# Optimization experiments

Hardware: AMD Instinct MI355X
Metric: run time of the kernel (lower is better)

Reference implementation:

```python
import jax, jax.numpy as jnp
import numpy as np
from jax import lax

LN_EPS = 1e-5

D_MODEL, N_HEADS, HEAD_DIM, RANK, POWER_K = 1024, 16, 64, 32, 4
RIDGE_EPS, SPECTRAL_GAMMA = 1e-4, 0.99


def setup_inputs() -> dict:
    key = jax.random.key(0)
    ks = jax.random.split(key, 8)
    B, T = 4, 4096
    s = 1.0 / np.sqrt(D_MODEL)
    inp = {
        "hidden_states": jax.random.normal(ks[0], (B, T, D_MODEL), dtype=jnp.float32),
        "Wk": jax.random.normal(ks[1], (D_MODEL, N_HEADS * RANK), dtype=jnp.float32) * s,
        "Wq": jax.random.normal(ks[2], (D_MODEL, N_HEADS * RANK), dtype=jnp.float32) * s,
        "Wv": jax.random.normal(ks[3], (D_MODEL, N_HEADS * HEAD_DIM), dtype=jnp.float32) * s,
        "Wo": jax.random.normal(ks[4], (N_HEADS * HEAD_DIM, D_MODEL), dtype=jnp.float32) * s,
        "ln_scale": jnp.ones((D_MODEL,), jnp.float32),
        "ln_bias": jnp.zeros((D_MODEL,), jnp.float32),
        "gate_alpha": jnp.zeros((1,), jnp.float32),
        "log_ridge": jnp.array(np.log(RIDGE_EPS), jnp.float32),
        "log_gamma": jnp.array(np.log(SPECTRAL_GAMMA), jnp.float32),
        "prefix_len": 2048,
    }
    return inp


def _tri_solve(L, b, transpose=False):
    # solves L x = b (or L^T x = b) with lower-triangular L; batched over leading dims
    return lax.linalg.triangular_solve(L, b, left_side=True, lower=True, transpose_a=transpose)


def _build_operator(keys, values, ridge, gamma):
    # keys: (B,H,L,r), values: (B,H,L,dh)
    r = keys.shape[-1]
    G = jnp.einsum('bhlr,bhls->bhrs', keys, keys) + ridge * jnp.eye(r, dtype=keys.dtype)
    M = jnp.einsum('bhlr,bhls->bhrs', keys[:, :, 1:, :], keys[:, :, :-1, :])
    L = jnp.linalg.cholesky(G)                       # (B,H,r,r)
    U = _tri_solve(L, M)                             # L^{-1} M
    V = _tri_solve(L, jnp.swapaxes(U, -1, -2))       # L^{-1} (L^{-1}M)^T
    A_w = jnp.swapaxes(V, -1, -2)                    # L^{-1} M L^{-T}
    gamma_c = jnp.minimum(gamma, 1.0)
    sigma = jnp.linalg.svd(A_w, compute_uv=False)[..., 0]  # spectral norm
    sigma = jnp.maximum(sigma, 1e-8)
    scale = gamma_c / jnp.maximum(sigma, 1.0)
    A_w = A_w * scale[..., None, None]
    C_v = jnp.einsum('bhld,bhlr->bhdr', values, keys)       # (B,H,dh,r)
    Y = _tri_solve(L, jnp.swapaxes(C_v, -1, -2))            # L^{-1} C_v^T
    Bv_T = _tri_solve(L, Y, transpose=True)                 # G^{-1} C_v^T
    B_v = jnp.swapaxes(Bv_T, -1, -2)                        # (B,H,dh,r)
    return A_w, L, B_v


def _spectral_filter(A_w, L, B_v, queries, power_K):
    # queries: (B,H,Q,r) -> (B,H,Q,dh)
    qT = jnp.swapaxes(queries, -1, -2)      # (B,H,r,Q)
    w = _tri_solve(L, qT)                   # whiten
    for _ in range(power_K):
        w = jnp.matmul(A_w, w)
    z_hat = jnp.matmul(L, w)                # unwhiten
    out = jnp.matmul(B_v, z_hat)            # (B,H,dh,Q)
    return jnp.swapaxes(out, -1, -2)


def reference(hidden_states, Wk, Wq, Wv, Wo, ln_scale, ln_bias,
              gate_alpha, log_ridge, log_gamma, prefix_len):
    B, T, D = hidden_states.shape
    P = max(1, min(int(prefix_len), T - 1))
    mu = jnp.mean(hidden_states, axis=-1, keepdims=True)
    var = jnp.var(hidden_states, axis=-1, keepdims=True)
    normed = (hidden_states - mu) / jnp.sqrt(var + LN_EPS) * ln_scale + ln_bias
    def proj(W, dim):
        y = normed @ W
        return jnp.swapaxes(y.reshape(B, T, N_HEADS, dim), 1, 2)  # (B,H,T,dim)
    keys_all = proj(Wk, RANK)
    queries_all = proj(Wq, RANK)
    values_all = proj(Wv, HEAD_DIM)
    ridge = jnp.exp(log_ridge)
    gamma = jnp.exp(log_gamma)
    A_w, L, B_v = _build_operator(keys_all[:, :, :P, :], values_all[:, :, :P, :], ridge, gamma)
    q_out = _spectral_filter(A_w, L, B_v, queries_all[:, :, P:, :], POWER_K)
    p_out = _spectral_filter(A_w, L, B_v, keys_all[:, :, :P, :], POWER_K)
    full = jnp.concatenate([p_out, q_out], axis=2)               # (B,H,T,dh)
    full = jnp.swapaxes(full, 1, 2).reshape(B, T, N_HEADS * HEAD_DIM)
    out = full @ Wo
    return jax.nn.sigmoid(gate_alpha) * out
```

## Files before the change

kernel.cpp:

```cpp
#include <hip/hip_runtime.h>
#include <math.h>

#define D_MODEL 1024
#define TT 4096
#define NB 4
#define NH 16
#define TCH 8

typedef __attribute__((ext_vector_type(8))) short s8v;
typedef __attribute__((ext_vector_type(4))) float f4v;
typedef __attribute__((ext_vector_type(8))) unsigned short u16x8;

#define OFF_STATS ((size_t)0)
#define OFF_GP    ((size_t)(1) << 20)
#define OFF_MP    ((size_t)(3) << 20)
#define OFF_CP    ((size_t)(5) << 20)
#define OFF_FT    ((size_t)(9) << 20)
#define OFF_WKH   ((size_t)(10) << 20)
#define OFF_WKL   ((size_t)(11) << 20)
#define OFF_WQH   ((size_t)(12) << 20)
#define OFF_WQL   ((size_t)(13) << 20)
#define OFF_WVH   ((size_t)(14) << 20)
#define OFF_WVL   ((size_t)(16) << 20)
#define OFF_WOH   ((size_t)(18) << 20)
#define OFF_WOL   ((size_t)(20) << 20)
#define OFF_Y1    ((size_t)(22) << 20)
#define OFF_Y2    ((size_t)(54) << 20)
#define OFF_FH    OFF_Y2

__device__ __forceinline__ unsigned short bf16_rne(float x) {
  unsigned u = __float_as_uint(x);
  return (unsigned short)((u + 0x7fffu + ((u >> 16) & 1u)) >> 16);
}
__device__ __forceinline__ void split_bf16(float x, unsigned short& h, unsigned short& l) {
  unsigned u = __float_as_uint(x);
  unsigned r = (u + 0x7fffu + ((u >> 16) & 1u)) & 0xffff0000u;
  h = (unsigned short)(r >> 16);
  float res = x - __uint_as_float(r);
  l = bf16_rne(res);
}

__device__ __forceinline__ void gll16(unsigned short* lds, const unsigned short* g) {
  __builtin_amdgcn_global_load_lds(
      (__attribute__((address_space(1))) void*)(void*)(g),
      (__attribute__((address_space(3))) void*)(lds), 16, 0, 0);
}

__device__ __forceinline__ void xcd_swz(int gx, int gy, int& x, int& y, int& z) {
  int wg = blockIdx.x + gx * (blockIdx.y + gy * blockIdx.z);
  int k = wg & 7, j = wg >> 3;
  x = j % gx;
  int yz = k + ((j / gx) << 3);
  y = yz % gy;
  z = yz / gy;
}

__global__ __launch_bounds__(256) void ln_stats_k(const float* __restrict__ X,
                                                  float* __restrict__ stats) {
  int r = blockIdx.x;
  const float4 v = ((const float4*)(X + (size_t)r * D_MODEL))[threadIdx.x];
  float s  = v.x + v.y + v.z + v.w;
  float ss = v.x * v.x + v.y * v.y + v.z * v.z + v.w * v.w;
#pragma unroll
  for (int off = 32; off > 0; off >>= 1) {
    s  += __shfl_down(s, off, 64);
    ss += __shfl_down(ss, off, 64);
  }
  __shared__ float as_[4], bs_[4];
  int w = threadIdx.x >> 6, lane = threadIdx.x & 63;
  if (lane == 0) { as_[w] = s; bs_[w] = ss; }
  __syncthreads();
  if (threadIdx.x == 0) {
    float S  = as_[0] + as_[1] + as_[2] + as_[3];
    float SS = bs_[0] + bs_[1] + bs_[2] + bs_[3];
    float mu  = S * (1.0f / D_MODEL);
    float var = SS * (1.0f / D_MODEL) - mu * mu;
    stats[2 * (size_t)r]     = mu;
    stats[2 * (size_t)r + 1] = 1.0f / sqrtf(var + 1e-5f);
  }
}

__global__ __launch_bounds__(256) void prep_w_k(const float* __restrict__ W, int N,
                                                unsigned short* __restrict__ Thi,
                                                unsigned short* __restrict__ Tlo,
                                                int swz) {
  __shared__ float tileT[32 * 33];
  const int n0 = blockIdx.x * 32, k0 = blockIdx.y * 32;
  const int tid = threadIdx.x;
  {
    int k_l = tid >> 3, n4 = (tid & 7) << 2;
    float4 v = *(const float4*)&W[(size_t)(k0 + k_l) * N + n0 + n4];
    tileT[(n4 + 0) * 33 + k_l] = v.x;
    tileT[(n4 + 1) * 33 + k_l] = v.y;
    tileT[(n4 + 2) * 33 + k_l] = v.z;
    tileT[(n4 + 3) * 33 + k_l] = v.w;
  }
  __syncthreads();
  {
    int n_l = tid >> 3, k4 = (tid & 7) << 2;
    unsigned short h[4], l[4];
#pragma unroll
    for (int i = 0; i < 4; i++) split_bf16(tileT[n_l * 33 + k4 + i], h[i], l[i]);
    int kc = k0 + k4;
    int col = swz ? ((kc & ~63) | ((((kc >> 3) & 7) ^ (n_l & 7)) << 3) | (kc & 7)) : kc;
    *(ushort4*)&Thi[(size_t)(n0 + n_l) * 1024 + col] = make_ushort4(h[0], h[1], h[2], h[3]);
    *(ushort4*)&Tlo[(size_t)(n0 + n_l) * 1024 + col] = make_ushort4(l[0], l[1], l[2], l[3]);
  }
}

__global__ __launch_bounds__(256) void gemm_proj_k(
    const float* __restrict__ X, const float* __restrict__ stats,
    const float* __restrict__ lng, const float* __restrict__ lnb,
    const unsigned short* __restrict__ WThi, const unsigned short* __restrict__ WTlo,
    int Nw, const int* __restrict__ pref, int mode, float* __restrict__ Y) {
  int P = pref[0]; P = P < 1 ? 1 : (P > TT - 1 ? TT - 1 : P);
  int xx, yy, zz;
  xcd_swz(8, 32, xx, yy, zz);
  const int b  = zz;
  const int t0 = yy * 128;
  const int n0 = xx * 128;
  if (mode == 1) { if (t0 + 128 <= P) return; }
  else           { if (t0 >= P) return; }
  const int row0 = b * TT + t0;
  __shared__ __align__(16) unsigned short Ah[128 * 40], Al[128 * 40];
  __shared__ __align__(16) unsigned short Bh[128 * 32], Bl[128 * 32];
  __shared__ float mus[128], rss[128];
  const int tid = threadIdx.x;
  if (tid < 128) {
    mus[tid] = stats[2 * (size_t)(row0 + tid)];
    rss[tid] = stats[2 * (size_t)(row0 + tid) + 1];
  }
  const int lane = tid & 63;
  const int wid  = tid >> 6;
  const int wm = (wid >> 1) * 64, wn = (wid & 1) * 64;
  const int lm = lane & 15, lq = lane >> 4;
  const int srow = lane >> 2, scol = (lane & 3) << 3;
  f4v acc[4][4];
#pragma unroll
  for (int i = 0; i < 4; i++)
#pragma unroll
    for (int j = 0; j < 4; j++) acc[i][j] = (f4v){0.f, 0.f, 0.f, 0.f};

  for (int kt = 0; kt < D_MODEL; kt += 32) {
    __syncthreads();
#pragma unroll
    for (int s = 0; s < 2; s++) {
      int seg = wid * 2 + s;
      int brow = n0 + seg * 16 + srow;
      gll16(&Bh[seg * 512], &WThi[(size_t)brow * 1024 + kt + scol]);
      gll16(&Bl[seg * 512], &WTlo[(size_t)brow * 1024 + kt + scol]);
    }
#pragma unroll
    for (int q = 0; q < 2; q++) {
      int c = tid * 2 + q;
      int m = c >> 2, k8 = (c & 3) << 3;
      const float* src = &X[(size_t)(row0 + m) * D_MODEL + kt + k8];
      float mu = mus[m], rs = rss[m];
      u16x8 hv, lv;
#pragma unroll
      for (int i = 0; i < 8; i++) {
        float nv = (src[i] - mu) * rs * lng[kt + k8 + i] + lnb[kt + k8 + i];
        unsigned short h, l;
        split_bf16(nv, h, l);
        hv[i] = h; lv[i] = l;
      }
      *(u16x8*)&Ah[m * 40 + k8] = hv;
      *(u16x8*)&Al[m * 40 + k8] = lv;
    }
    __syncthreads();
    s8v ah[4], al[4], bh[4], bl[4];
#pragma unroll
    for (int i = 0; i < 4; i++) {
      int ar = (wm + i * 16 + lm) * 40 + lq * 8;
      int br = (wn + i * 16 + lm) * 32 + lq * 8;
      ah[i] = *(const s8v*)&Ah[ar];
      al[i] = *(const s8v*)&Al[ar];
      bh[i] = *(const s8v*)&Bh[br];
      bl[i] = *(const s8v*)&Bl[br];
    }
#pragma unroll
    for (int mi = 0; mi < 4; mi++)
#pragma unroll
      for (int ni = 0; ni < 4; ni++) {
        acc[mi][ni] = __builtin_amdgcn_mfma_f32_16x16x32_bf16(ah[mi], bh[ni], acc[mi][ni], 0, 0, 0);
        acc[mi][ni] = __builtin_amdgcn_mfma_f32_16x16x32_bf16(ah[mi], bl[ni], acc[mi][ni], 0, 0, 0);
        acc[mi][ni] = __builtin_amdgcn_mfma_f32_16x16x32_bf16(al[mi], bh[ni], acc[mi][ni], 0, 0, 0);
      }
  }
#pragma unroll
  for (int mi = 0; mi < 4; mi++) {
#pragma unroll
    for (int r = 0; r < 4; r++) {
      int t = t0 + wm + mi * 16 + lq * 4 + r;
      bool ok = (mode == 1) ? (t >= P) : (t < P);
      if (!ok) continue;
      size_t orow = (mode == 2) ? ((size_t)b * P + t) : ((size_t)b * TT + t);
#pragma unroll
      for (int ni = 0; ni < 4; ni++)
        Y[orow * Nw + n0 + wn + ni * 16 + lm] = acc[mi][ni][r];
    }
  }
}

__global__ __launch_bounds__(256) void gemm_kq_k(
    const float* __restrict__ X, const float* __restrict__ stats,
    const float* __restrict__ lng, const float* __restrict__ lnb,
    const unsigned short* __restrict__ KH, const unsigned short* __restrict__ KL,
    const unsigned short* __restrict__ QH, const unsigned short* __restrict__ QL,
    const int* __restrict__ pref, float* __restrict__ Y) {
  int P = pref[0]; P = P < 1 ? 1 : (P > TT - 1 ? TT - 1 : P);
  int xx, yy, zz;
  xcd_swz(4, 32, xx, yy, zz);
  const int b  = zz;
  const int t0 = yy * 128;
  const int n0 = xx * 128;
  const int row0 = b * TT + t0;
  const bool hasK = (t0 < P);
  const bool hasQ = (t0 + 128 > P);
  __shared__ __align__(16) unsigned short Ah[128 * 40], Al[128 * 40];
  __shared__ __align__(16) unsigned short Bh[128 * 32], Bl[128 * 32];
  __shared__ float mus[128], rss[128];
  const int tid = threadIdx.x;
  if (tid < 128) {
    mus[tid] = stats[2 * (size_t)(row0 + tid)];
    rss[tid] = stats[2 * (size_t)(row0 + tid) + 1];
  }
  const int lane = tid & 63;
  const int wid  = tid >> 6;
  const int wm = (wid >> 1) * 64, wn = (wid & 1) * 64;
  const int lm = lane & 15, lq = lane >> 4;
  const int srow = lane >> 2, scol = (lane & 3) << 3;

  for (int pass = 0; pass < 2; pass++) {
    if (pass == 0 && !hasK) continue;
    if (pass == 1 && !hasQ) continue;
    const unsigned short* WThi = pass ? QH : KH;
    const unsigned short* WTlo = pass ? QL : KL;
    f4v acc[4][4];
#pragma unroll
    for (int i = 0; i < 4; i++)
#pragma unroll
      for (int j = 0; j < 4; j++) acc[i][j] = (f4v){0.f, 0.f, 0.f, 0.f};

    for (int kt = 0; kt < D_MODEL; kt += 32) {
      __syncthreads();
#pragma unroll
      for (int s = 0; s < 2; s++) {
        int seg = wid * 2 + s;
        int brow = n0 + seg * 16 + srow;
        gll16(&Bh[seg * 512], &WThi[(size_t)brow * 1024 + kt + scol]);
        gll16(&Bl[seg * 512], &WTlo[(size_t)brow * 1024 + kt + scol]);
      }
#pragma unroll
      for (int q = 0; q < 2; q++) {
        int c = tid * 2 + q;
        int m = c >> 2, k8 = (c & 3) << 3;
        const float* src = &X[(size_t)(row0 + m) * D_MODEL + kt + k8];
        float mu = mus[m], rs = rss[m];
        u16x8 hv, lv;
#pragma unroll
        for (int i = 0; i < 8; i++) {
          float nv = (src[i] - mu) * rs * lng[kt + k8 + i] + lnb[kt + k8 + i];
          unsigned short h, l;
          split_bf16(nv, h, l);
          hv[i] = h; lv[i] = l;
        }
        *(u16x8*)&Ah[m * 40 + k8] = hv;
        *(u16x8*)&Al[m * 40 + k8] = lv;
      }
      __syncthreads();
      s8v ah[4], al[4], bh[4], bl[4];
#pragma unroll
      for (int i = 0; i < 4; i++) {
        int ar = (wm + i * 16 + lm) * 40 + lq * 8;
        int br = (wn + i * 16 + lm) * 32 + lq * 8;
        ah[i] = *(const s8v*)&Ah[ar];
        al[i] = *(const s8v*)&Al[ar];
        bh[i] = *(const s8v*)&Bh[br];
        bl[i] = *(const s8v*)&Bl[br];
      }
#pragma unroll
      for (int mi = 0; mi < 4; mi++)
#pragma unroll
        for (int ni = 0; ni < 4; ni++) {
          acc[mi][ni] = __builtin_amdgcn_mfma_f32_16x16x32_bf16(ah[mi], bh[ni], acc[mi][ni], 0, 0, 0);
          acc[mi][ni] = __builtin_amdgcn_mfma_f32_16x16x32_bf16(ah[mi], bl[ni], acc[mi][ni], 0, 0, 0);
          acc[mi][ni] = __builtin_amdgcn_mfma_f32_16x16x32_bf16(al[mi], bh[ni], acc[mi][ni], 0, 0, 0);
        }
    }
#pragma unroll
    for (int mi = 0; mi < 4; mi++) {
#pragma unroll
      for (int r = 0; r < 4; r++) {
        int t = t0 + wm + mi * 16 + lq * 4 + r;
        bool ok = pass ? (t >= P) : (t < P);
        if (!ok) continue;
#pragma unroll
        for (int ni = 0; ni < 4; ni++)
          Y[((size_t)b * TT + t) * 512 + n0 + wn + ni * 16 + lm] = acc[mi][ni][r];
      }
    }
  }
}

__global__ __launch_bounds__(256) void build_gmc_mfma_k(
    const float* __restrict__ Y1, const float* __restrict__ Y2,
    const int* __restrict__ pref,
    float* __restrict__ Gp, float* __restrict__ Mp, float* __restrict__ Cp) {
  int P = pref[0]; P = P < 1 ? 1 : (P > TT - 1 ? TT - 1 : P);
  const int c  = blockIdx.x;
  const int bh = blockIdx.y;
  const int b = bh >> 4, h = bh & 15;
  const int chunk = (P + TCH - 1) / TCH;
  const int tb = c * chunk;
  const int te = min(tb + chunk, P);

  __shared__ __align__(16) unsigned short kCh[32 * 136], kCl[32 * 136];
  __shared__ __align__(16) unsigned short kPh[32 * 136], kPl[32 * 136];
  __shared__ __align__(16) unsigned short vTh[64 * 136], vTl[64 * 136];

  const int tid = threadIdx.x;
  const int wid = tid >> 6, lane = tid & 63;
  const int lm = lane & 15, lq = lane >> 4;

  f4v acc[4];
#pragma unroll
  for (int i = 0; i < 4; i++) acc[i] = (f4v){0.f, 0.f, 0.f, 0.f};

  for (int t0 = tb; t0 < te; t0 += 128) {
    const int len = (te - t0 < 128) ? (te - t0) : 128;
    __syncthreads();
    for (int e = tid; e < 129 * 8; e += 256) {
      int row = e >> 3, j4 = (e & 7) << 2;
      int t = t0 - 1 + row;
      float4 kv = make_float4(0.f, 0.f, 0.f, 0.f);
      if (row <= len && t >= 0)
        kv = *(const float4*)&Y1[((size_t)b * TT + t) * 512 + h * 32 + j4];
      unsigned short hh[4], ll[4];
      split_bf16(kv.x, hh[0], ll[0]); split_bf16(kv.y, hh[1], ll[1]);
      split_bf16(kv.z, hh[2], ll[2]); split_bf16(kv.w, hh[3], ll[3]);
      if (row >= 1) {
#pragma unroll
        for (int q = 0; q < 4; q++) {
          kCh[(j4 + q) * 136 + row - 1] = hh[q];
          kCl[(j4 + q) * 136 + row - 1] = ll[q];
        }
      }
      if (row < 128) {
#pragma unroll
        for (int q = 0; q < 4; q++) {
          kPh[(j4 + q) * 136 + row] = hh[q];
          kPl[(j4 + q) * 136 + row] = ll[q];
        }
      }
    }
    for (int e = tid; e < 128 * 16; e += 256) {
      int row = e >> 4, dj = (e & 15) << 2;
      int t = t0 + row;
      float4 vv = make_float4(0.f, 0.f, 0.f, 0.f);
      if (row < len)
        vv = *(const float4*)&Y2[((size_t)b * P + t) * 1024 + h * 64 + dj];
      unsigned short hh[4], ll[4];
      split_bf16(vv.x, hh[0], ll[0]); split_bf16(vv.y, hh[1], ll[1]);
      split_bf16(vv.z, hh[2], ll[2]); split_bf16(vv.w, hh[3], ll[3]);
#pragma unroll
      for (int q = 0; q < 4; q++) {
        vTh[(dj + q) * 136 + row] = hh[q];
        vTl[(dj + q) * 136 + row] = ll[q];
      }
    }
    __syncthreads();

#pragma unroll
    for (int kk = 0; kk < 128; kk += 32) {
      const int off = kk + lq * 8;
      if (wid == 0) {
        s8v h0 = *(const s8v*)&kCh[(0 + lm) * 136 + off];
        s8v h1 = *(const s8v*)&kCh[(16 + lm) * 136 + off];
        s8v l0 = *(const s8v*)&kCl[(0 + lm) * 136 + off];
        s8v l1 = *(const s8v*)&kCl[(16 + lm) * 136 + off];
        acc[0] = __builtin_amdgcn_mfma_f32_16x16x32_bf16(h0, h0, acc[0], 0, 0, 0);
        acc[0] = __builtin_amdgcn_mfma_f32_16x16x32_bf16(h0, l0, acc[0], 0, 0, 0);
        acc[0] = __builtin_amdgcn_mfma_f32_16x16x32_bf16(l0, h0, acc[0], 0, 0, 0);
        acc[1] = __builtin_amdgcn_mfma_f32_16x16x32_bf16(h0, h1, acc[1], 0, 0, 0);
        acc[1] = __builtin_amdgcn_mfma_f32_16x16x32_bf16(h0, l1, acc[1], 0, 0, 0);
        acc[1] = __builtin_amdgcn_mfma_f32_16x16x32_bf16(l0, h1, acc[1], 0, 0, 0);
        acc[2] = __builtin_amdgcn_mfma_f32_16x16x32_bf16(h1, h0, acc[2], 0, 0, 0);
        acc[2] = __builtin_amdgcn_mfma_f32_16x16x32_bf16(h1, l0, acc[2], 0, 0, 0);
        acc[2] = __builtin_amdgcn_mfma_f32_16x16x32_bf16(l1, h0, acc[2], 0, 0, 0);
        acc[3] = __builtin_amdgcn_mfma_f32_16x16x32_bf16(h1, h1, acc[3], 0, 0, 0);
        acc[3] = __builtin_amdgcn_mfma_f32_16x16x32_bf16(h1, l1, acc[3], 0, 0, 0);
        acc[3] = __builtin_amdgcn_mfma_f32_16x16x32_bf16(l1, h1, acc[3], 0, 0, 0);
      } else if (wid == 1) {
        s8v ah0 = *(const s8v*)&kCh[(0 + lm) * 136 + off];
        s8v ah1 = *(const s8v*)&kCh[(16 + lm) * 136 + off];
        s8v al0 = *(const s8v*)&kCl[(0 + lm) * 136 + off];
        s8v al1 = *(const s8v*)&kCl[(16 + lm) * 136 + off];
        s8v bh0 = *(const s8v*)&kPh[(0 + lm) * 136 + off];
        s8v bh1 = *(const s8v*)&kPh[(16 + lm) * 136 + off];
        s8v bl0 = *(const s8v*)&kPl[(0 + lm) * 136 + off];
        s8v bl1 = *(const s8v*)&kPl[(16 + lm) * 136 + off];
        acc[0] = __builtin_amdgcn_mfma_f32_16x16x32_bf16(ah0, bh0, acc[0], 0, 0, 0);
        acc[0] = __builtin_amdgcn_mfma_f32_16x16x32_bf16(ah0, bl0, acc[0], 0, 0, 0);
        acc[0] = __builtin_amdgcn_mfma_f32_16x16x32_bf16(al0, bh0, acc[0], 0, 0, 0);
        acc[1] = __builtin_amdgcn_mfma_f32_16x16x32_bf16(ah0, bh1, acc[1], 0, 0, 0);
        acc[1] = __builtin_amdgcn_mfma_f32_16x16x32_bf16(ah0, bl1, acc[1], 0, 0, 0);
        acc[1] = __builtin_amdgcn_mfma_f32_16x16x32_bf16(al0, bh1, acc[1], 0, 0, 0);
        acc[2] = __builtin_amdgcn_mfma_f32_16x16x32_bf16(ah1, bh0, acc[2], 0, 0, 0);
        acc[2] = __builtin_amdgcn_mfma_f32_16x16x32_bf16(ah1, bl0, acc[2], 0, 0, 0);
        acc[2] = __builtin_amdgcn_mfma_f32_16x16x32_bf16(al1, bh0, acc[2], 0, 0, 0);
        acc[3] = __builtin_amdgcn_mfma_f32_16x16x32_bf16(ah1, bh1, acc[3], 0, 0, 0);
        acc[3] = __builtin_amdgcn_mfma_f32_16x16x32_bf16(ah1, bl1, acc[3], 0, 0, 0);
        acc[3] = __builtin_amdgcn_mfma_f32_16x16x32_bf16(al1, bh1, acc[3], 0, 0, 0);
      } else {
        const int d0 = (wid - 2) * 32;
        s8v vh0 = *(const s8v*)&vTh[(d0 + lm) * 136 + off];
        s8v vh1 = *(const s8v*)&vTh[(d0 + 16 + lm) * 136 + off];
        s8v vl0 = *(const s8v*)&vTl[(d0 + lm) * 136 + off];
        s8v vl1 = *(const s8v*)&vTl[(d0 + 16 + lm) * 136 + off];
        s8v kh0 = *(const s8v*)&kCh[(0 + lm) * 136 + off];
        s8v kh1 = *(const s8v*)&kCh[(16 + lm) * 136 + off];
        s8v kl0 = *(const s8v*)&kCl[(0 + lm) * 136 + off];
        s8v kl1 = *(const s8v*)&kCl[(16 + lm) * 136 + off];
        acc[0] = __builtin_amdgcn_mfma_f32_16x16x32_bf16(vh0, kh0, acc[0], 0, 0, 0);
        acc[0] = __builtin_amdgcn_mfma_f32_16x16x32_bf16(vh0, kl0, acc[0], 0, 0, 0);
        acc[0] = __builtin_amdgcn_mfma_f32_16x16x32_bf16(vl0, kh0, acc[0], 0, 0, 0);
        acc[1] = __builtin_amdgcn_mfma_f32_16x16x32_bf16(vh0, kh1, acc[1], 0, 0, 0);
        acc[1] = __builtin_amdgcn_mfma_f32_16x16x32_bf16(vh0, kl1, acc[1], 0, 0, 0);
        acc[1] = __builtin_amdgcn_mfma_f32_16x16x32_bf16(vl0, kh1, acc[1], 0, 0, 0);
        acc[2] = __builtin_amdgcn_mfma_f32_16x16x32_bf16(vh1, kh0, acc[2], 0, 0, 0);
        acc[2] = __builtin_amdgcn_mfma_f32_16x16x32_bf16(vh1, kl0, acc[2], 0, 0, 0);
        acc[2] = __builtin_amdgcn_mfma_f32_16x16x32_bf16(vl1, kh0, acc[2], 0, 0, 0);
        acc[3] = __builtin_amdgcn_mfma_f32_16x16x32_bf16(vh1, kh1, acc[3], 0, 0, 0);
        acc[3] = __builtin_amdgcn_mfma_f32_16x16x32_bf16(vh1, kl1, acc[3], 0, 0, 0);
        acc[3] = __builtin_amdgcn_mfma_f32_16x16x32_bf16(vl1, kh1, acc[3], 0, 0, 0);
      }
    }
  }

  if (wid < 2) {
    float* dst = (wid == 0 ? Gp : Mp) + (size_t)(c * 64 + bh) * 1024;
#pragma unroll
    for (int t = 0; t < 4; t++) {
      int i0 = (t >> 1) * 16, j0 = (t & 1) * 16;
#pragma unroll
      for (int r = 0; r < 4; r++)
        dst[(i0 + lq * 4 + r) * 32 + j0 + lm] = acc[t][r];
    }
  } else {
    float* dst = Cp + (size_t)(c * 64 + bh) * 2048;
#pragma unroll
    for (int t = 0; t < 4; t++) {
      int d0 = (wid - 2) * 32 + (t >> 1) * 16, j0 = (t & 1) * 16;
#pragma unroll
      for (int r = 0; r < 4; r++)
        dst[(d0 + lq * 4 + r) * 32 + j0 + lm] = acc[t][r];
    }
  }
}

__global__ __launch_bounds__(256) void solve_op_k(
    const float* __restrict__ Gp, const float* __restrict__ Mp,
    const float* __restrict__ Cp, const float* __restrict__ lridge,
    const float* __restrict__ lgamma, float* __restrict__ Ft) {
  __shared__ float Gs[32 * 33];
  __shared__ float Ms[32 * 32];
  __shared__ float Gi[32 * 32];
  __shared__ float W1[32 * 33];
  __shared__ float Aw[32 * 33];
  __shared__ float Nn[32 * 32];
  __shared__ float N2[32 * 32];
  __shared__ float T1[32 * 32];
  __shared__ float Cs[64 * 32];
  __shared__ float red[256];
  __shared__ float vv[32], uu[32];
  const int bh = blockIdx.x;
  const int tid = threadIdx.x;
  const float ridge = expf(lridge[0]);

  for (int e = tid; e < 1024; e += 256) {
    int i = e >> 5, j = e & 31;
    float g = 0.f, m = 0.f;
#pragma unroll
    for (int cc = 0; cc < TCH; cc++) {
      g += Gp[(size_t)(cc * 64 + bh) * 1024 + e];
      m += Mp[(size_t)(cc * 64 + bh) * 1024 + e];
    }
    if (i == j) g += ridge;
    Gs[i * 33 + j] = g;
    Ms[e] = m;
  }
  for (int e = tid; e < 2048; e += 256) {
    float s = 0.f;
#pragma unroll
    for (int cc = 0; cc < TCH; cc++) s += Cp[(size_t)(cc * 64 + bh) * 2048 + e];
    Cs[e] = s;
  }
  __syncthreads();

  for (int j = 0; j < 32; j++) {
    float d = Gs[j * 33 + j];
    __syncthreads();
    float inv = 1.0f / sqrtf(d);
    if (tid >= j && tid < 32) Gs[tid * 33 + j] *= inv;
    __syncthreads();
    int w = 31 - j;
    for (int e = tid; e < w * w; e += 256) {
      int i = j + 1 + e / w, k = j + 1 + e % w;
      Gs[i * 33 + k] -= Gs[i * 33 + j] * Gs[k * 33 + j];
    }
    __syncthreads();
  }

  if (tid < 32) {
    const int c = tid;
    for (int i = 0; i < 32; i++) W1[i * 33 + c] = (i == c) ? 1.0f : 0.0f;
    for (int i = 0; i < 32; i++) {
      float s = W1[i * 33 + c];
      for (int j = 0; j < i; j++) s -= Gs[i * 33 + j] * W1[j * 33 + c];
      W1[i * 33 + c] = s / Gs[i * 33 + i];
    }
    for (int i = 31; i >= 0; i--) {
      float s = W1[i * 33 + c];
      for (int j = i + 1; j < 32; j++) s -= Gs[j * 33 + i] * W1[j * 33 + c];
      W1[i * 33 + c] = s / Gs[i * 33 + i];
    }
    for (int i = 0; i < 32; i++) Gi[i * 32 + c] = W1[i * 33 + c];
  }
  __syncthreads();
  if (tid < 32) {
    const int c = tid;
    for (int i = 0; i < 32; i++) {
      float s = Ms[i * 32 + c];
      for (int j = 0; j < i; j++) s -= Gs[i * 33 + j] * W1[j * 33 + c];
      W1[i * 33 + c] = s / Gs[i * 33 + i];
    }
  }
  __syncthreads();
  if (tid < 32) {
    const int c = tid;
    for (int i = 0; i < 32; i++) {
      float s = W1[c * 33 + i];
      for (int j = 0; j < i; j++) s -= Gs[i * 33 + j] * Aw[j * 33 + c];
      Aw[i * 33 + c] = s / Gs[i * 33 + i];
    }
  }
  __syncthreads();

  float s0 = 0.0f;
  for (int e = tid; e < 1024; e += 256) {
    float a = Aw[(e >> 5) * 33 + (e & 31)];
    s0 += a * a;
  }
  red[tid] = s0;
  __syncthreads();
  for (int off = 128; off > 0; off >>= 1) {
    if (tid < off) red[tid] += red[tid + off];
    __syncthreads();
  }
  float frob2 = red[0];
  float sigma;
  if (frob2 <= 1.0f) {
    sigma = sqrtf(frob2);
  } else {
    if (tid < 32) vv[tid] = 1.0f + 0.001f * (float)tid;
    __syncthreads();
    for (int it = 0; it < 64; it++) {
      if (tid < 32) {
        float s = 0;
        for (int j = 0; j < 32; j++) s += Aw[tid * 33 + j] * vv[j];
        uu[tid] = s;
      }
      __syncthreads();
      if (tid == 0) {
        float n = 0;
        for (int j = 0; j < 32; j++) n += uu[j] * uu[j];
        red[0] = sqrtf(n);
      }
      __syncthreads();
      float nu = fmaxf(red[0], 1e-30f);
      if (tid < 32) uu[tid] /= nu;
      __syncthreads();
      if (tid < 32) {
        float s = 0;
        for (int j = 0; j < 32; j++) s += Aw[j * 33 + tid] * uu[j];
        vv[tid] = s;
      }
      __syncthreads();
      if (tid == 0) {
        float n = 0;
        for (int j = 0; j < 32; j++) n += vv[j] * vv[j];
        red[0] = sqrtf(n);
      }
      __syncthreads();
      float nv = fmaxf(red[0], 1e-30f);
      if (tid < 32) vv[tid] /= nv;
      __syncthreads();
    }
    sigma = red[0];
  }
  float gamma_c = fminf(expf(lgamma[0]), 1.0f);
  float scale = gamma_c / fmaxf(fmaxf(sigma, 1e-8f), 1.0f);

  for (int e = tid; e < 1024; e += 256) {
    int i = e >> 5, c = e & 31;
    float s = 0;
#pragma unroll
    for (int k = 0; k < 32; k++) s += Ms[i * 32 + k] * Gi[k * 32 + c];
    Nn[e] = scale * s;
  }
  __syncthreads();
  for (int e = tid; e < 1024; e += 256) {
    int i = e >> 5, c = e & 31;
    float s = 0;
#pragma unroll
    for (int k = 0; k < 32; k++) s += Nn[i * 32 + k] * Nn[k * 32 + c];
    N2[e] = s;
  }
  __syncthreads();
  for (int e = tid; e < 1024; e += 256) {
    int i = e >> 5, c = e & 31;
    float s = 0;
#pragma unroll
    for (int k = 0; k < 32; k++) s += N2[i * 32 + k] * N2[k * 32 + c];
    Ms[e] = s;
  }
  __syncthreads();
  for (int e = tid; e < 1024; e += 256) {
    int i = e >> 5, c = e & 31;
    float s = 0;
#pragma unroll
    for (int k = 0; k < 32; k++) s += Gi[i * 32 + k] * Ms[k * 32 + c];
    T1[e] = s;
  }
  __syncthreads();
  for (int e = tid; e < 2048; e += 256) {
    int j = e >> 6, d = e & 63;
    float s = 0;
#pragma unroll
    for (int k = 0; k < 32; k++) s += Cs[d * 32 + k] * T1[k * 32 + j];
    Ft[(size_t)bh * 2048 + e] = s;
  }
}

__global__ __launch_bounds__(256) void apply_k(const float* __restrict__ Y1,
                                               const float* __restrict__ Ft,
                                               unsigned short* __restrict__ FH) {
  __shared__ float xs[128 * 32];
  const int h = blockIdx.y;
  const int r0 = blockIdx.x * 128;
  const int bh = (r0 >> 12) * NH + h;
  const int tid = threadIdx.x;
  const int d = tid & 63, t0 = tid >> 6;
  float fcol[32];
  const float* fb = &Ft[(size_t)bh * 2048 + d];
#pragma unroll
  for (int j = 0; j < 32; j++) fcol[j] = fb[j * 64];
  for (int e = tid; e < 1024; e += 256) {
    int row = e >> 3, j4 = (e & 7) << 2;
    *(float4*)&xs[row * 32 + j4] =
        *(const float4*)&Y1[((size_t)(r0 + row)) * 512 + h * 32 + j4];
  }
  __syncthreads();
  const int dq = d >> 3, dr = d & 7;
  for (int tl = t0; tl < 128; tl += 4) {
    float s = 0;
#pragma unroll
    for (int j = 0; j < 32; j++) s += xs[tl * 32 + j] * fcol[j];
    int col = h * 64 + ((dq ^ (tl & 7)) << 3) + dr;
    FH[((size_t)(r0 + tl)) * 1024 + col] = bf16_rne(s);
  }
}

__global__ __launch_bounds__(512) void gemm_out_k(
    const unsigned short* __restrict__ FH,
    const unsigned short* __restrict__ WThi, const unsigned short* __restrict__ WTlo,
    const float* __restrict__ alpha, float* __restrict__ out) {
  __shared__ __align__(16) unsigned short lds[65536];
  int xx, yy, zz;
  xcd_swz(8, 64, xx, yy, zz);
  const int m0 = yy * 256;
  const int n0 = xx * 128;
  const int tid = threadIdx.x;
  const int lane = tid & 63;
  const int wid  = tid >> 6;
  const int wm = (wid >> 1) * 64;
  const int wn = (wid & 1) * 64;
  const int lm = lane & 15, lq = lane >> 4;
  const int l8 = lane >> 3, c8 = (lane & 7) << 3;

  f4v acc[4][4];
#pragma unroll
  for (int i = 0; i < 4; i++)
#pragma unroll
    for (int j = 0; j < 4; j++) acc[i][j] = (f4v){0.f, 0.f, 0.f, 0.f};

  auto STAGE = [&](int t, int buf) {
    const int kt = t * 64;
#pragma unroll
    for (int i = 0; i < 4; i++) {
      int iss = wid * 4 + i;
      gll16(&lds[buf * 16384 + iss * 512],
            &FH[(size_t)(m0 + iss * 8 + l8) * 1024 + kt + c8]);
    }
#pragma unroll
    for (int i = 0; i < 2; i++) {
      int iss = wid * 2 + i;
      gll16(&lds[32768 + buf * 8192 + iss * 512],
            &WThi[(size_t)(n0 + iss * 8 + l8) * 1024 + kt + c8]);
    }
#pragma unroll
    for (int i = 0; i < 2; i++) {
      int iss = wid * 2 + i;
      gll16(&lds[49152 + buf * 8192 + iss * 512],
            &WTlo[(size_t)(n0 + iss * 8 + l8) * 1024 + kt + c8]);
    }
  };

  STAGE(0, 0);
  STAGE(1, 1);

  for (int t = 0; t < 16; t++) {
    const int buf = t & 1;
    if (t < 15) asm volatile("s_waitcnt vmcnt(8)" ::: "memory");
    else        asm volatile("s_waitcnt vmcnt(0)" ::: "memory");
    __builtin_amdgcn_s_barrier();
    const unsigned short* Ab  = &lds[buf * 16384];
    const unsigned short* Bhb = &lds[32768 + buf * 8192];
    const unsigned short* Blb = &lds[49152 + buf * 8192];
    __builtin_amdgcn_s_setprio(1);
#pragma unroll
    for (int kk = 0; kk < 2; kk++) {
      s8v ah[4], bh[4], bl[4];
#pragma unroll
      for (int i = 0; i < 4; i++) {
        int rA = wm + i * 16 + lm;
        int rB = wn + i * 16 + lm;
        int sA = (((kk * 4 + lq) ^ (rA & 7)) << 3);
        int sB = (((kk * 4 + lq) ^ (rB & 7)) << 3);
        ah[i] = *(const s8v*)&Ab[rA * 64 + sA];
        bh[i] = *(const s8v*)&Bhb[rB * 64 + sB];
        bl[i] = *(const s8v*)&Blb[rB * 64 + sB];
      }
#pragma unroll
      for (int mi = 0; mi < 4; mi++)
#pragma unroll
        for (int ni = 0; ni < 4; ni++) {
          acc[mi][ni] = __builtin_amdgcn_mfma_f32_16x16x32_bf16(ah[mi], bh[ni], acc[mi][ni], 0, 0, 0);
          acc[mi][ni] = __builtin_amdgcn_mfma_f32_16x16x32_bf16(ah[mi], bl[ni], acc[mi][ni], 0, 0, 0);
        }
    }
    __builtin_amdgcn_s_setprio(0);
    __builtin_amdgcn_sched_barrier(0);
    __builtin_amdgcn_s_barrier();
    if (t < 14) STAGE(t + 2, buf);
  }

  float sg = 1.0f / (1.0f + expf(-alpha[0]));
#pragma unroll
  for (int mi = 0; mi < 4; mi++)
#pragma unroll
    for (int r = 0; r < 4; r++) {
      size_t orow = (size_t)(m0 + wm + mi * 16 + lq * 4 + r);
#pragma unroll
      for (int ni = 0; ni < 4; ni++)
        out[orow * 1024 + n0 + wn + ni * 16 + lm] = sg * acc[mi][ni][r];
    }
}

extern "C" void kernel_launch(void* const* d_in, const int* in_sizes, int n_in,
                              void* d_out, int out_size, void* d_ws, size_t ws_size,
                              hipStream_t stream) {
  const float* X      = (const float*)d_in[0];
  const float* Wk     = (const float*)d_in[1];
  const float* Wq     = (const float*)d_in[2];
  const float* Wv     = (const float*)d_in[3];
  const float* Wo     = (const float*)d_in[4];
  const float* lng    = (const float*)d_in[5];
  const float* lnb    = (const float*)d_in[6];
  const float* alpha  = (const float*)d_in[7];
  const float* lridge = (const float*)d_in[8];
  const float* lgamma = (const float*)d_in[9];
  const int*   pref   = (const int*)d_in[10];
  float* out = (float*)d_out;
  char* ws = (char*)d_ws;
  float* stats = (float*)(ws + OFF_STATS);
  float* Gp    = (float*)(ws + OFF_GP);
  float* Mp    = (float*)(ws + OFF_MP);
  float* Cp    = (float*)(ws + OFF_CP);
  float* Ft    = (float*)(ws + OFF_FT);
  unsigned short* WKH = (unsigned short*)(ws + OFF_WKH);
  unsigned short* WKL = (unsigned short*)(ws + OFF_WKL);
  unsigned short* WQH = (unsigned short*)(ws + OFF_WQH);
  unsigned short* WQL = (unsigned short*)(ws + OFF_WQL);
  unsigned short* WVH = (unsigned short*)(ws + OFF_WVH);
  unsigned short* WVL = (unsigned short*)(ws + OFF_WVL);
  unsigned short* WOH = (unsigned short*)(ws + OFF_WOH);
  unsigned short* WOL = (unsigned short*)(ws + OFF_WOL);
  float* Y1 = (float*)(ws + OFF_Y1);
  float* Y2 = (float*)(ws + OFF_Y2);
  unsigned short* FH = (unsigned short*)(ws + OFF_FH);

  ln_stats_k<<<16384, 256, 0, stream>>>(X, stats);
  prep_w_k<<<dim3(16, 32), 256, 0, stream>>>(Wk, 512, WKH, WKL, 0);
  prep_w_k<<<dim3(16, 32), 256, 0, stream>>>(Wq, 512, WQH, WQL, 0);
  prep_w_k<<<dim3(32, 32), 256, 0, stream>>>(Wv, 1024, WVH, WVL, 0);
  prep_w_k<<<dim3(32, 32), 256, 0, stream>>>(Wo, 1024, WOH, WOL, 1);
  gemm_kq_k<<<dim3(4, 32, NB), 256, 0, stream>>>(X, stats, lng, lnb, WKH, WKL, WQH, WQL, pref, Y1);
  gemm_proj_k<<<dim3(8, 32, NB), 256, 0, stream>>>(X, stats, lng, lnb, WVH, WVL, 1024, pref, 2, Y2);
  build_gmc_mfma_k<<<dim3(TCH, 64), 256, 0, stream>>>(Y1, Y2, pref, Gp, Mp, Cp);
  solve_op_k<<<64, 256, 0, stream>>>(Gp, Mp, Cp, lridge, lgamma, Ft);
  apply_k<<<dim3(128, NH), 256, 0, stream>>>(Y1, Ft, FH);
  gemm_out_k<<<dim3(8, 64), 512, 0, stream>>>(FH, WOH, WOL, alpha, out);
}
```

Measured before the change: 461.8 us.

## Widen projection GEMM tiles to 128x256 and use wave-level power iteration

```diff
diff --git a/kernel.cpp b/kernel.cpp
--- a/kernel.cpp
+++ b/kernel.cpp
@@ -108,22 +108,22 @@
   }
 }
 
-__global__ __launch_bounds__(256) void gemm_proj_k(
+__global__ __launch_bounds__(512) void gemm_proj_k(
     const float* __restrict__ X, const float* __restrict__ stats,
     const float* __restrict__ lng, const float* __restrict__ lnb,
     const unsigned short* __restrict__ WThi, const unsigned short* __restrict__ WTlo,
     int Nw, const int* __restrict__ pref, int mode, float* __restrict__ Y) {
   int P = pref[0]; P = P < 1 ? 1 : (P > TT - 1 ? TT - 1 : P);
   int xx, yy, zz;
-  xcd_swz(8, 32, xx, yy, zz);
+  xcd_swz(4, 32, xx, yy, zz);
   const int b  = zz;
   const int t0 = yy * 128;
-  const int n0 = xx * 128;
+  const int n0 = xx * 256;
   if (mode == 1) { if (t0 + 128 <= P) return; }
   else           { if (t0 >= P) return; }
   const int row0 = b * TT + t0;
   __shared__ __align__(16) unsigned short Ah[128 * 40], Al[128 * 40];
-  __shared__ __align__(16) unsigned short Bh[128 * 32], Bl[128 * 32];
+  __shared__ __align__(16) unsigned short Bh[256 * 32], Bl[256 * 32];
   __shared__ float mus[128], rss[128];
   const int tid = threadIdx.x;
   if (tid < 128) {
@@ -132,7 +132,7 @@
   }
   const int lane = tid & 63;
   const int wid  = tid >> 6;
-  const int wm = (wid >> 1) * 64, wn = (wid & 1) * 64;
+  const int wm = (wid >> 2) * 64, wn = (wid & 3) * 64;
   const int lm = lane & 15, lq = lane >> 4;
   const int srow = lane >> 2, scol = (lane & 3) << 3;
   f4v acc[4][4];
@@ -150,10 +150,8 @@
       gll16(&Bh[seg * 512], &WThi[(size_t)brow * 1024 + kt + scol]);
       gll16(&Bl[seg * 512], &WTlo[(size_t)brow * 1024 + kt + scol]);
     }
-#pragma unroll
-    for (int q = 0; q < 2; q++) {
-      int c = tid * 2 + q;
-      int m = c >> 2, k8 = (c & 3) << 3;
+    {
+      int m = tid >> 2, k8 = (tid & 3) << 3;
       const float* src = &X[(size_t)(row0 + m) * D_MODEL + kt + k8];
       float mu = mus[m], rs = rss[m];
       u16x8 hv, lv;
@@ -202,7 +200,7 @@
   }
 }
 
-__global__ __launch_bounds__(256) void gemm_kq_k(
+__global__ __launch_bounds__(512) void gemm_kq_k(
     const float* __restrict__ X, const float* __restrict__ stats,
     const float* __restrict__ lng, const float* __restrict__ lnb,
     const unsigned short* __restrict__ KH, const unsigned short* __restrict__ KL,
@@ -210,15 +208,15 @@
     const int* __restrict__ pref, float* __restrict__ Y) {
   int P = pref[0]; P = P < 1 ? 1 : (P > TT - 1 ? TT - 1 : P);
   int xx, yy, zz;
-  xcd_swz(4, 32, xx, yy, zz);
+  xcd_swz(2, 32, xx, yy, zz);
   const int b  = zz;
   const int t0 = yy * 128;
-  const int n0 = xx * 128;
+  const int n0 = xx * 256;
   const int row0 = b * TT + t0;
   const bool hasK = (t0 < P);
   const bool hasQ = (t0 + 128 > P);
   __shared__ __align__(16) unsigned short Ah[128 * 40], Al[128 * 40];
-  __shared__ __align__(16) unsigned short Bh[128 * 32], Bl[128 * 32];
+  __shared__ __align__(16) unsigned short Bh[256 * 32], Bl[256 * 32];
   __shared__ float mus[128], rss[128];
   const int tid = threadIdx.x;
   if (tid < 128) {
@@ -227,7 +225,7 @@
   }
   const int lane = tid & 63;
   const int wid  = tid >> 6;
-  const int wm = (wid >> 1) * 64, wn = (wid & 1) * 64;
+  const int wm = (wid >> 2) * 64, wn = (wid & 3) * 64;
   const int lm = lane & 15, lq = lane >> 4;
   const int srow = lane >> 2, scol = (lane & 3) << 3;
 
@@ -251,10 +249,8 @@
         gll16(&Bh[seg * 512], &WThi[(size_t)brow * 1024 + kt + scol]);
         gll16(&Bl[seg * 512], &WTlo[(size_t)brow * 1024 + kt + scol]);
       }
-#pragma unroll
-      for (int q = 0; q < 2; q++) {
-        int c = tid * 2 + q;
-        int m = c >> 2, k8 = (c & 3) << 3;
+      {
+        int m = tid >> 2, k8 = (tid & 3) << 3;
         const float* src = &X[(size_t)(row0 + m) * D_MODEL + kt + k8];
         float mu = mus[m], rs = rss[m];
         u16x8 hv, lv;
@@ -473,7 +469,6 @@
   __shared__ float T1[32 * 32];
   __shared__ float Cs[64 * 32];
   __shared__ float red[256];
-  __shared__ float vv[32], uu[32];
   const int bh = blockIdx.x;
   const int tid = threadIdx.x;
   const float ridge = expf(lridge[0]);
@@ -563,40 +558,36 @@
   if (frob2 <= 1.0f) {
     sigma = sqrtf(frob2);
   } else {
-    if (tid < 32) vv[tid] = 1.0f + 0.001f * (float)tid;
-    __syncthreads();
-    for (int it = 0; it < 64; it++) {
-      if (tid < 32) {
-        float s = 0;
-        for (int j = 0; j < 32; j++) s += Aw[tid * 33 + j] * vv[j];
-        uu[tid] = s;
-      }
-      __syncthreads();
-      if (tid == 0) {
-        float n = 0;
-        for (int j = 0; j < 32; j++) n += uu[j] * uu[j];
-        red[0] = sqrtf(n);
-      }
-      __syncthreads();
-      float nu = fmaxf(red[0], 1e-30f);
-      if (tid < 32) uu[tid] /= nu;
-      __syncthreads();
-      if (tid < 32) {
-        float s = 0;
-        for (int j = 0; j < 32; j++) s += Aw[j * 33 + tid] * uu[j];
-        vv[tid] = s;
-      }
-      __syncthreads();
-      if (tid == 0) {
-        float n = 0;
-        for (int j = 0; j < 32; j++) n += vv[j] * vv[j];
-        red[0] = sqrtf(n);
-      }
-      __syncthreads();
-      float nv = fmaxf(red[0], 1e-30f);
-      if (tid < 32) vv[tid] /= nv;
-      __syncthreads();
-    }
+    __syncthreads();
+    if (tid < 64) {
+      const int i = tid & 31;
+      float ar[32], at[32];
+#pragma unroll
+      for (int j = 0; j < 32; j++) { ar[j] = Aw[i * 33 + j]; at[j] = Aw[j * 33 + i]; }
+      float v = 1.0f + 0.001f * (float)i;
+      float sig = 0.0f, prev = -1.0f;
+      for (int it = 0; it < 64; it++) {
+        float u = 0.0f;
+#pragma unroll
+        for (int j = 0; j < 32; j++) u += ar[j] * __shfl(v, j, 64);
+        float nu2 = u * u;
+#pragma unroll
+        for (int off = 16; off > 0; off >>= 1) nu2 += __shfl_xor(nu2, off, 64);
+        u /= fmaxf(sqrtf(nu2), 1e-30f);
+        float vn = 0.0f;
+#pragma unroll
+        for (int j = 0; j < 32; j++) vn += at[j] * __shfl(u, j, 64);
+        float nv2 = vn * vn;
+#pragma unroll
+        for (int off = 16; off > 0; off >>= 1) nv2 += __shfl_xor(nv2, off, 64);
+        sig = sqrtf(nv2);
+        v = vn / fmaxf(sig, 1e-30f);
+        if (it >= 7 && fabsf(sig - prev) <= 1e-7f * sig) break;
+        prev = sig;
+      }
+      if (tid == 0) red[0] = sig;
+    }
+    __syncthreads();
     sigma = red[0];
   }
   float gamma_c = fminf(expf(lgamma[0]), 1.0f);
@@ -806,8 +797,8 @@
   prep_w_k<<<dim3(16, 32), 256, 0, stream>>>(Wq, 512, WQH, WQL, 0);
   prep_w_k<<<dim3(32, 32), 256, 0, stream>>>(Wv, 1024, WVH, WVL, 0);
   prep_w_k<<<dim3(32, 32), 256, 0, stream>>>(Wo, 1024, WOH, WOL, 1);
-  gemm_kq_k<<<dim3(4, 32, NB), 256, 0, stream>>>(X, stats, lng, lnb, WKH, WKL, WQH, WQL, pref, Y1);
-  gemm_proj_k<<<dim3(8, 32, NB), 256, 0, stream>>>(X, stats, lng, lnb, WVH, WVL, 1024, pref, 2, Y2);
+  gemm_kq_k<<<dim3(2, 32, NB), 512, 0, stream>>>(X, stats, lng, lnb, WKH, WKL, WQH, WQL, pref, Y1);
+  gemm_proj_k<<<dim3(4, 32, NB), 512, 0, stream>>>(X, stats, lng, lnb, WVH, WVL, 1024, pref, 2, Y2);
   build_gmc_mfma_k<<<dim3(TCH, 64), 256, 0, stream>>>(Y1, Y2, pref, Gp, Mp, Cp);
   solve_op_k<<<64, 256, 0, stream>>>(Gp, Mp, Cp, lridge, lgamma, Ft);
   apply_k<<<dim3(128, NH), 256, 0, stream>>>(Y1, Ft, FH);
```

New measurement: 474.2 us. 2.7% more time.
